# Optimization experiments

Hardware: AMD Instinct MI355X
Metric: run time of the kernel (lower is better)

The kernel has to match this reference:

```python
import jax, jax.numpy as jnp
import numpy as np

B, N, D, C = 256, 2000, 512, 100


def setup_inputs() -> dict:
    key = jax.random.key(0)
    k1, k2, k3, k4 = jax.random.split(key, 4)
    inputs = jax.random.normal(k1, (B, D), dtype=jnp.float32)
    support_tensors = jax.random.normal(k2, (N, D), dtype=jnp.float32)
    label_idx = jax.random.randint(k3, (N,), 0, C)
    support_labels = jax.nn.one_hot(label_idx, C, dtype=jnp.float32)
    kernel_w = jax.random.normal(k4, (D,), dtype=jnp.float32) * 0.05
    kernel_b = jnp.zeros((), dtype=jnp.float32)
    return {
        "inputs": inputs,
        "support_tensors": support_tensors,
        "support_labels": support_labels,
        "kernel_w": kernel_w,
        "kernel_b": kernel_b,
    }


def reference(inputs, support_tensors, support_labels, kernel_w, kernel_b):
    # Pairwise Cartesian product (batch x support): |a - b|, shape [B, N, D]
    diff = jnp.abs(inputs[:, None, :] - support_tensors[None, :, :])
    # Siamese kernel: sigmoid(Dense(1)(|a-b|)) -> scores [B, N]
    pair_wise_scores = jax.nn.sigmoid(jnp.einsum("bnd,d->bn", diff, kernel_w) + kernel_b)
    # Per-class aggregation: matmul with one-hot labels, then mean per class
    class_sums = pair_wise_scores @ support_labels  # [B, C]
    class_counts = jnp.sum(support_labels, axis=0)  # [C]
    # tf.math.divide_no_nan semantics
    return jnp.where(class_counts != 0, class_sums / class_counts, 0.0)
```

## Files before the change

### kernel.cpp

```cpp
#include <hip/hip_runtime.h>
#include <hip/hip_bf16.h>

#define B_SZ 256
#define N_SZ 2000
#define N_PAD 2048
#define D_SZ 512
#define C_SZ 100
#define BT 4
#define DC 8
#define NH 2
#define ZSPLIT 8
#define D4 (D_SZ / 4)

__global__ void prep_kernel(const float* __restrict__ labels,
                            int* __restrict__ idx) {
    int n = blockIdx.x * 256 + threadIdx.x;
    if (n < N_SZ) {
        const float4* row = (const float4*)(labels + (size_t)n * C_SZ);
        int c = 0;
#pragma unroll
        for (int j = 0; j < C_SZ / 4; ++j) {
            float4 v = row[j];
            if (v.x > 0.5f) c = 4 * j + 0;
            if (v.y > 0.5f) c = 4 * j + 1;
            if (v.z > 0.5f) c = 4 * j + 2;
            if (v.w > 0.5f) c = 4 * j + 3;
        }
        idx[n] = c;
    }
}

__global__ void transpose_kernel(const float4* __restrict__ sup4,
                                 float4* __restrict__ supT4) {
    int t = blockIdx.x * 256 + threadIdx.x;
    int dc = t >> 11;
    int n  = t & (N_PAD - 1);
    float4 v = make_float4(0.f, 0.f, 0.f, 0.f);
    if (n < N_SZ) v = sup4[(size_t)n * D4 + dc];
    supT4[t] = v;
}

__global__ __launch_bounds__(256, 2) void score_kernel(
    const float4* __restrict__ inp4,
    const float4* __restrict__ supT4,
    const float4* __restrict__ w4,
    float* __restrict__ S)
{
    int tid = threadIdx.x;
    int b0  = blockIdx.x * BT;
    float* __restrict__ Sp0 =
        S + ((size_t)blockIdx.y * B_SZ + b0) * N_PAD + tid;

#pragma unroll 1
    for (int h = 0; h < NH; ++h) {
        int dq = blockIdx.y * (NH * DC) + h * DC;

        unsigned vz = 0;
        asm volatile("" : "+v"(vz));

        float4 af[BT][DC];
        float4 wf[DC];
#pragma unroll
        for (int i = 0; i < BT; ++i) {
            const float4* __restrict__ ab = inp4 + (size_t)(b0 + i) * D4 + dq + vz;
#pragma unroll
            for (int j = 0; j < DC; ++j) af[i][j] = ab[j];
        }
        {
            const float4* __restrict__ wb = w4 + dq + vz;
#pragma unroll
            for (int j = 0; j < DC; ++j) wf[j] = wb[j];
        }

        const float4* __restrict__ sp = supT4 + (size_t)dq * N_PAD + tid;

        float4 sv[DC], nx[DC];
#pragma unroll
        for (int j = 0; j < DC; ++j) sv[j] = sp[(size_t)j * N_PAD];

#pragma unroll 1
        for (int n0 = 0; n0 < N_PAD - 256; n0 += 256) {
#pragma unroll
            for (int j = 0; j < DC; ++j)
                nx[j] = sp[(size_t)j * N_PAD + (n0 + 256)];

            float acc[BT] = {0.f, 0.f, 0.f, 0.f};
#pragma unroll
            for (int j = 0; j < DC; ++j) {
#pragma unroll
                for (int i = 0; i < BT; ++i) {
                    acc[i] += wf[j].x * fabsf(af[i][j].x - sv[j].x);
                    acc[i] += wf[j].y * fabsf(af[i][j].y - sv[j].y);
                    acc[i] += wf[j].z * fabsf(af[i][j].z - sv[j].z);
                    acc[i] += wf[j].w * fabsf(af[i][j].w - sv[j].w);
                }
            }

            float* Sp = Sp0 + n0;
            if (h == 0) {
#pragma unroll
                for (int i = 0; i < BT; ++i) Sp[(size_t)i * N_PAD] = acc[i];
            } else {
#pragma unroll
                for (int i = 0; i < BT; ++i) Sp[(size_t)i * N_PAD] += acc[i];
            }
#pragma unroll
            for (int j = 0; j < DC; ++j) sv[j] = nx[j];
        }

        {
            float acc[BT] = {0.f, 0.f, 0.f, 0.f};
#pragma unroll
            for (int j = 0; j < DC; ++j) {
#pragma unroll
                for (int i = 0; i < BT; ++i) {
                    acc[i] += wf[j].x * fabsf(af[i][j].x - sv[j].x);
                    acc[i] += wf[j].y * fabsf(af[i][j].y - sv[j].y);
                    acc[i] += wf[j].z * fabsf(af[i][j].z - sv[j].z);
                    acc[i] += wf[j].w * fabsf(af[i][j].w - sv[j].w);
                }
            }
            float* Sp = Sp0 + (N_PAD - 256);
            if (h == 0) {
#pragma unroll
                for (int i = 0; i < BT; ++i) Sp[(size_t)i * N_PAD] = acc[i];
            } else {
#pragma unroll
                for (int i = 0; i < BT; ++i) Sp[(size_t)i * N_PAD] += acc[i];
            }
        }
    }
}

__global__ void agg_kernel(const float* __restrict__ S,
                           const int* __restrict__ idx,
                           const float* __restrict__ bias_p,
                           float* __restrict__ out) {
    __shared__ float sums[C_SZ];
    __shared__ float cnts[C_SZ];
    int b = blockIdx.x;
    int t = threadIdx.x;
    if (t < C_SZ) { sums[t] = 0.f; cnts[t] = 0.f; }
    __syncthreads();
    float bias = *bias_p;
    for (int n = t; n < N_SZ; n += 256) {
        float logit = bias;
#pragma unroll
        for (int z = 0; z < ZSPLIT; ++z)
            logit += S[((size_t)z * B_SZ + b) * N_PAD + n];
        float s = 1.0f / (1.0f + __expf(-logit));
        int c = idx[n];
        atomicAdd(&sums[c], s);
        atomicAdd(&cnts[c], 1.0f);
    }
    __syncthreads();
    if (t < C_SZ) {
        float cnt = cnts[t];
        out[(size_t)b * C_SZ + t] = (cnt != 0.f) ? sums[t] / cnt : 0.f;
    }
}

extern "C" void kernel_launch(void* const* d_in, const int* in_sizes, int n_in,
                              void* d_out, int out_size, void* d_ws, size_t ws_size,
                              hipStream_t stream) {
    const float* inputs  = (const float*)d_in[0];
    const float* support = (const float*)d_in[1];
    const float* labels  = (const float*)d_in[2];
    const float* w       = (const float*)d_in[3];
    const float* bias    = (const float*)d_in[4];
    float* out = (float*)d_out;

    int*    idx   = (int*)d_ws;
    float4* supT4 = (float4*)((char*)d_ws + 16384);
    float*  S     = (float*)((char*)d_ws + 16384 + (size_t)D4 * N_PAD * sizeof(float4));

    prep_kernel<<<dim3((N_SZ + 255) / 256), dim3(256), 0, stream>>>(labels, idx);

    transpose_kernel<<<dim3(D4 * N_PAD / 256), dim3(256), 0, stream>>>(
        (const float4*)support, supT4);

    dim3 grid(B_SZ / BT, ZSPLIT);
    score_kernel<<<grid, dim3(256), 0, stream>>>(
        (const float4*)inputs, supT4, (const float4*)w, S);

    agg_kernel<<<dim3(B_SZ), dim3(256), 0, stream>>>(S, idx, bias, out);
}
```

Baseline: 46.66 us.

## Compute pairwise scores in packed fp16 with fdot2 and rebalance split

```diff
diff --git a/kernel.cpp b/kernel.cpp
--- a/kernel.cpp
+++ b/kernel.cpp
@@ -1,5 +1,4 @@
 #include <hip/hip_runtime.h>
-#include <hip/hip_bf16.h>
 
 #define B_SZ 256
 #define N_SZ 2000
@@ -7,129 +6,155 @@
 #define D_SZ 512
 #define C_SZ 100
 #define BT 4
-#define DC 8
-#define NH 2
-#define ZSPLIT 8
+#define JW 4
+#define ZSPLIT 16
 #define D4 (D_SZ / 4)
-
-__global__ void prep_kernel(const float* __restrict__ labels,
-                            int* __restrict__ idx) {
-    int n = blockIdx.x * 256 + threadIdx.x;
+#define DC8 (D_SZ / 8)
+
+typedef __fp16 h2 __attribute__((ext_vector_type(2)));
+
+struct alignas(16) H8 { h2 x, y, z, w; };
+struct alignas(8)  H4 { h2 lo, hi; };
+
+static __device__ __forceinline__ h2 habs2(h2 v) {
+    unsigned u = __builtin_bit_cast(unsigned, v) & 0x7FFF7FFFu;
+    return __builtin_bit_cast(h2, u);
+}
+
+#if __has_builtin(__builtin_amdgcn_fdot2)
+static __device__ __forceinline__ float DOT2(h2 d, h2 wv, float c) {
+    return __builtin_amdgcn_fdot2(d, wv, c, false);
+}
+#else
+static __device__ __forceinline__ float DOT2(h2 d, h2 wv, float c) {
+    return c + (float)d.x * (float)wv.x + (float)d.y * (float)wv.y;
+}
+#endif
+
+__global__ void setup_kernel(const float* __restrict__ labels,
+                             const float* __restrict__ inputs,
+                             const float* __restrict__ w,
+                             int* __restrict__ idx,
+                             H4* __restrict__ inpH4,
+                             __fp16* __restrict__ wH) {
+    int bid = blockIdx.x, tid = threadIdx.x;
+    if (bid < 8) {
+        int n = bid * 256 + tid;
+        if (n < N_SZ) {
+            const float4* row = (const float4*)(labels + (size_t)n * C_SZ);
+            int c = 0;
+#pragma unroll
+            for (int j = 0; j < C_SZ / 4; ++j) {
+                float4 v = row[j];
+                if (v.x > 0.5f) c = 4 * j + 0;
+                if (v.y > 0.5f) c = 4 * j + 1;
+                if (v.z > 0.5f) c = 4 * j + 2;
+                if (v.w > 0.5f) c = 4 * j + 3;
+            }
+            idx[n] = c;
+        }
+    } else if (bid == 8) {
+        wH[tid]       = (__fp16)w[tid];
+        wH[tid + 256] = (__fp16)w[tid + 256];
+    } else {
+        int i4 = (bid - 9) * 256 + tid;
+        float4 v = ((const float4*)inputs)[i4];
+        H4 o;
+        o.lo = __builtin_amdgcn_cvt_pkrtz(v.x, v.y);
+        o.hi = __builtin_amdgcn_cvt_pkrtz(v.z, v.w);
+        inpH4[i4] = o;
+    }
+}
+
+__global__ void transposeH_kernel(const float4* __restrict__ sup4,
+                                  H8* __restrict__ supH) {
+    int t = blockIdx.x * 256 + threadIdx.x;
+    int dc8 = t >> 11;
+    int n   = t & (N_PAD - 1);
+    H8 o = {};
     if (n < N_SZ) {
-        const float4* row = (const float4*)(labels + (size_t)n * C_SZ);
-        int c = 0;
-#pragma unroll
-        for (int j = 0; j < C_SZ / 4; ++j) {
-            float4 v = row[j];
-            if (v.x > 0.5f) c = 4 * j + 0;
-            if (v.y > 0.5f) c = 4 * j + 1;
-            if (v.z > 0.5f) c = 4 * j + 2;
-            if (v.w > 0.5f) c = 4 * j + 3;
-        }
-        idx[n] = c;
-    }
-}
-
-__global__ void transpose_kernel(const float4* __restrict__ sup4,
-                                 float4* __restrict__ supT4) {
-    int t = blockIdx.x * 256 + threadIdx.x;
-    int dc = t >> 11;
-    int n  = t & (N_PAD - 1);
-    float4 v = make_float4(0.f, 0.f, 0.f, 0.f);
-    if (n < N_SZ) v = sup4[(size_t)n * D4 + dc];
-    supT4[t] = v;
-}
-
-__global__ __launch_bounds__(256, 2) void score_kernel(
-    const float4* __restrict__ inp4,
-    const float4* __restrict__ supT4,
-    const float4* __restrict__ w4,
+        float4 p = sup4[(size_t)n * D4 + 2 * dc8];
+        float4 q = sup4[(size_t)n * D4 + 2 * dc8 + 1];
+        o.x = __builtin_amdgcn_cvt_pkrtz(p.x, p.y);
+        o.y = __builtin_amdgcn_cvt_pkrtz(p.z, p.w);
+        o.z = __builtin_amdgcn_cvt_pkrtz(q.x, q.y);
+        o.w = __builtin_amdgcn_cvt_pkrtz(q.z, q.w);
+    }
+    supH[t] = o;
+}
+
+__global__ __launch_bounds__(256, 3) void score_kernel(
+    const H8* __restrict__ inpH8,
+    const H8* __restrict__ supH,
+    const H8* __restrict__ wH8,
     float* __restrict__ S)
 {
     int tid = threadIdx.x;
     int b0  = blockIdx.x * BT;
-    float* __restrict__ Sp0 =
-        S + ((size_t)blockIdx.y * B_SZ + b0) * N_PAD + tid;
+    int dc0 = blockIdx.y * JW;
+
+    unsigned vz = 0;
+    asm volatile("" : "+v"(vz));
+
+    H8 af[BT][JW];
+    H8 wf[JW];
+#pragma unroll
+    for (int i = 0; i < BT; ++i) {
+        const H8* ap = inpH8 + (size_t)(b0 + i) * DC8 + dc0 + vz;
+#pragma unroll
+        for (int j = 0; j < JW; ++j) af[i][j] = ap[j];
+    }
+    {
+        const H8* wp = wH8 + dc0 + vz;
+#pragma unroll
+        for (int j = 0; j < JW; ++j) wf[j] = wp[j];
+    }
+
+    const H8* sp0 = supH + (size_t)(dc0 + 0) * N_PAD + tid;
+    const H8* sp1 = supH + (size_t)(dc0 + 1) * N_PAD + tid;
+    const H8* sp2 = supH + (size_t)(dc0 + 2) * N_PAD + tid;
+    const H8* sp3 = supH + (size_t)(dc0 + 3) * N_PAD + tid;
+
+    float* Sp0 = S + ((size_t)blockIdx.y * B_SZ + b0) * N_PAD + tid;
+
+#define STEP(J, SV)                                                  \
+    {                                                                \
+        H8 wv = wf[J];                                               \
+        _Pragma("unroll") for (int i = 0; i < BT; ++i) {             \
+            H8 a = af[i][J];                                         \
+            acc[i] = DOT2(habs2(a.x - SV.x), wv.x, acc[i]);          \
+            acc[i] = DOT2(habs2(a.y - SV.y), wv.y, acc[i]);          \
+            acc[i] = DOT2(habs2(a.z - SV.z), wv.z, acc[i]);          \
+            acc[i] = DOT2(habs2(a.w - SV.w), wv.w, acc[i]);          \
+        }                                                            \
+    }
+
+    H8 sv0 = sp0[0], sv1 = sp1[0], sv2 = sp2[0], sv3 = sp3[0];
 
 #pragma unroll 1
-    for (int h = 0; h < NH; ++h) {
-        int dq = blockIdx.y * (NH * DC) + h * DC;
-
-        unsigned vz = 0;
-        asm volatile("" : "+v"(vz));
-
-        float4 af[BT][DC];
-        float4 wf[DC];
-#pragma unroll
-        for (int i = 0; i < BT; ++i) {
-            const float4* __restrict__ ab = inp4 + (size_t)(b0 + i) * D4 + dq + vz;
-#pragma unroll
-            for (int j = 0; j < DC; ++j) af[i][j] = ab[j];
-        }
-        {
-            const float4* __restrict__ wb = w4 + dq + vz;
-#pragma unroll
-            for (int j = 0; j < DC; ++j) wf[j] = wb[j];
-        }
-
-        const float4* __restrict__ sp = supT4 + (size_t)dq * N_PAD + tid;
-
-        float4 sv[DC], nx[DC];
-#pragma unroll
-        for (int j = 0; j < DC; ++j) sv[j] = sp[(size_t)j * N_PAD];
-
-#pragma unroll 1
-        for (int n0 = 0; n0 < N_PAD - 256; n0 += 256) {
-#pragma unroll
-            for (int j = 0; j < DC; ++j)
-                nx[j] = sp[(size_t)j * N_PAD + (n0 + 256)];
-
-            float acc[BT] = {0.f, 0.f, 0.f, 0.f};
-#pragma unroll
-            for (int j = 0; j < DC; ++j) {
-#pragma unroll
-                for (int i = 0; i < BT; ++i) {
-                    acc[i] += wf[j].x * fabsf(af[i][j].x - sv[j].x);
-                    acc[i] += wf[j].y * fabsf(af[i][j].y - sv[j].y);
-                    acc[i] += wf[j].z * fabsf(af[i][j].z - sv[j].z);
-                    acc[i] += wf[j].w * fabsf(af[i][j].w - sv[j].w);
-                }
-            }
-
-            float* Sp = Sp0 + n0;
-            if (h == 0) {
-#pragma unroll
-                for (int i = 0; i < BT; ++i) Sp[(size_t)i * N_PAD] = acc[i];
-            } else {
-#pragma unroll
-                for (int i = 0; i < BT; ++i) Sp[(size_t)i * N_PAD] += acc[i];
-            }
-#pragma unroll
-            for (int j = 0; j < DC; ++j) sv[j] = nx[j];
-        }
-
-        {
-            float acc[BT] = {0.f, 0.f, 0.f, 0.f};
-#pragma unroll
-            for (int j = 0; j < DC; ++j) {
-#pragma unroll
-                for (int i = 0; i < BT; ++i) {
-                    acc[i] += wf[j].x * fabsf(af[i][j].x - sv[j].x);
-                    acc[i] += wf[j].y * fabsf(af[i][j].y - sv[j].y);
-                    acc[i] += wf[j].z * fabsf(af[i][j].z - sv[j].z);
-                    acc[i] += wf[j].w * fabsf(af[i][j].w - sv[j].w);
-                }
-            }
-            float* Sp = Sp0 + (N_PAD - 256);
-            if (h == 0) {
-#pragma unroll
-                for (int i = 0; i < BT; ++i) Sp[(size_t)i * N_PAD] = acc[i];
-            } else {
-#pragma unroll
-                for (int i = 0; i < BT; ++i) Sp[(size_t)i * N_PAD] += acc[i];
-            }
-        }
-    }
+    for (int n0 = 0; n0 < N_PAD - 256; n0 += 256) {
+        float acc[BT] = {0.f, 0.f, 0.f, 0.f};
+        H8 nx0 = sp0[n0 + 256];
+        STEP(0, sv0);
+        H8 nx1 = sp1[n0 + 256];
+        STEP(1, sv1);
+        H8 nx2 = sp2[n0 + 256];
+        STEP(2, sv2);
+        H8 nx3 = sp3[n0 + 256];
+        STEP(3, sv3);
+#pragma unroll
+        for (int i = 0; i < BT; ++i)
+            Sp0[(size_t)i * N_PAD + n0] = acc[i];
+        sv0 = nx0; sv1 = nx1; sv2 = nx2; sv3 = nx3;
+    }
+    {
+        float acc[BT] = {0.f, 0.f, 0.f, 0.f};
+        STEP(0, sv0); STEP(1, sv1); STEP(2, sv2); STEP(3, sv3);
+#pragma unroll
+        for (int i = 0; i < BT; ++i)
+            Sp0[(size_t)i * N_PAD + (N_PAD - 256)] = acc[i];
+    }
+#undef STEP
 }
 
 __global__ void agg_kernel(const float* __restrict__ S,
@@ -143,7 +168,7 @@
     if (t < C_SZ) { sums[t] = 0.f; cnts[t] = 0.f; }
     __syncthreads();
     float bias = *bias_p;
-    for (int n = t; n < N_SZ; n += 256) {
+    for (int n = t; n < N_SZ; n += 512) {
         float logit = bias;
 #pragma unroll
         for (int z = 0; z < ZSPLIT; ++z)
@@ -170,18 +195,21 @@
     const float* bias    = (const float*)d_in[4];
     float* out = (float*)d_out;
 
-    int*    idx   = (int*)d_ws;
-    float4* supT4 = (float4*)((char*)d_ws + 16384);
-    float*  S     = (float*)((char*)d_ws + 16384 + (size_t)D4 * N_PAD * sizeof(float4));
-
-    prep_kernel<<<dim3((N_SZ + 255) / 256), dim3(256), 0, stream>>>(labels, idx);
-
-    transpose_kernel<<<dim3(D4 * N_PAD / 256), dim3(256), 0, stream>>>(
-        (const float4*)support, supT4);
+    int*     idx  = (int*)d_ws;
+    __fp16*  wH   = (__fp16*)((char*)d_ws + 8192);
+    __fp16*  inpH = (__fp16*)((char*)d_ws + 16384);
+    H8*      supH = (H8*)((char*)d_ws + 524288);
+    float*   S    = (float*)((char*)d_ws + 4 * 1024 * 1024);
+
+    setup_kernel<<<dim3(9 + B_SZ * D_SZ / 4 / 256), dim3(256), 0, stream>>>(
+        labels, inputs, w, idx, (H4*)inpH, wH);
+
+    transposeH_kernel<<<dim3(DC8 * N_PAD / 256), dim3(256), 0, stream>>>(
+        (const float4*)support, supH);
 
     dim3 grid(B_SZ / BT, ZSPLIT);
     score_kernel<<<grid, dim3(256), 0, stream>>>(
-        (const float4*)inputs, supT4, (const float4*)w, S);
-
-    agg_kernel<<<dim3(B_SZ), dim3(256), 0, stream>>>(S, idx, bias, out);
-}
+        (const H8*)inpH, supH, (const H8*)wH, S);
+
+    agg_kernel<<<dim3(B_SZ), dim3(512), 0, stream>>>(S, idx, bias, out);
+}
```

After: 42.07 us. -9.8%, faster.
